# Optimization experiments

Measured on AMD Instinct MI355X. Metric: run time of the kernel, lower is better.

Reference implementation:

```python
import jax, jax.numpy as jnp
import numpy as np

NEURON_CDECAY = 0.5
NEURON_VDECAY = 0.75
NEURON_VTH = 0.5

B, D_IN, T = 4096, 1024, 16
H1, H2, D_OUT = 1024, 1024, 512


def setup_inputs() -> dict:
    key = jax.random.key(0)
    ks = jax.random.split(key, 7)
    def lin(k, fan_in, shape):
        bound = 1.0 / np.sqrt(fan_in)
        return jax.random.uniform(k, shape, jnp.float32, -bound, bound)
    # input spikes: binary-ish spike trains in [0,1)
    in_pop_spikes = (jax.random.uniform(ks[0], (B, D_IN, T)) < 0.3).astype(jnp.float32)
    return {
        "in_pop_spikes": in_pop_spikes,
        "W1": lin(ks[1], D_IN, (H1, D_IN)), "b1": lin(ks[2], D_IN, (H1,)),
        "W2": lin(ks[3], H1, (H2, H1)), "b2": lin(ks[4], H1, (H2,)),
        "Wo": lin(ks[5], H2, (D_OUT, H2)), "bo": lin(ks[6], H2, (D_OUT,)),
        "batch_size": B,
    }


def pseudo_spike(volt):
    return (volt > NEURON_VTH).astype(volt.dtype)


def clif_step(x, W, b, cur, volt, spk):
    cur = cur * NEURON_CDECAY + x @ W.T + b
    volt = volt * NEURON_VDECAY * (1.0 - spk) + cur
    spk = pseudo_spike(volt)
    return cur, volt, spk


def reference(in_pop_spikes, W1, b1, W2, b2, Wo, bo, batch_size):
    bsz = batch_size
    xs = jnp.transpose(in_pop_spikes, (2, 0, 1))  # [T, B, D_in]
    z = lambda d: jnp.zeros((bsz, d), jnp.float32)
    init = (z(H1), z(H1), z(H1), z(H2), z(H2), z(H2), z(D_OUT), z(D_OUT), z(D_OUT))

    def step(state, x):
        c1, v1, s1, c2, v2, s2, co, vo, so = state
        c1, v1, s1 = clif_step(x, W1, b1, c1, v1, s1)
        c2, v2, s2 = clif_step(s1, W2, b2, c2, v2, s2)
        co, vo, so = clif_step(s2, Wo, bo, co, vo, so)
        return (c1, v1, s1, c2, v2, s2, co, vo, so), so

    _, spikes = jax.lax.scan(step, init, xs)  # spikes: [T, B, D_out]
    return jnp.sum(spikes, axis=0) / T
```

## Files before the change

### kernel.cpp

```cpp
#include <hip/hip_runtime.h>


static constexpr int BSZ   = 4096;
static constexpr int D_IN  = 1024;
static constexpr int H1    = 1024;
static constexpr int D_OUT = 512;
static constexpr int M_ROWS = BSZ * 16;

__global__ void pack_x(const float* __restrict__ X, float* __restrict__ A) {
    const int P = blockIdx.x * 256 + threadIdx.x;
    const int b = P >> 10, d = P & 1023;
    const float4* xp = (const float4*)(X + (size_t)P * 16);
    float4 x0 = xp[0], x1 = xp[1], x2 = xp[2], x3 = xp[3];
    const float v[16] = {x0.x, x0.y, x0.z, x0.w, x1.x, x1.y, x1.z, x1.w,
                         x2.x, x2.y, x2.z, x2.w, x3.x, x3.y, x3.z, x3.w};
#pragma unroll
    for (int t = 0; t < 16; ++t)
        A[((size_t)(b * 16 + t)) * 1024 + d] = v[t];
}

__global__ __launch_bounds__(256, 2) void gemm_np(
    const float* __restrict__ A,
    const float* __restrict__ W,
    float* __restrict__ C,
    int N) {
#pragma clang fp contract(off)
    __shared__ float As[32][128];
    __shared__ float Ws[32][128];

    const int tid = threadIdx.x;
    const int tx = tid & 15;
    const int ty = tid >> 4;
    const int m0 = blockIdx.x * 128, n0 = blockIdx.y * 128;

    const int arow = tid & 127, akh = tid >> 7;

    const float* Ab = A + (size_t)(m0 + arow) * 1024 + akh * 16;
    const float* Wb = W + (size_t)(n0 + arow) * 1024 + akh * 16;

    float pacc[8][8] = {};

    for (int kt = 0; kt < 32; ++kt) {
        const int k0 = kt * 32;
        float4 av0 = *(const float4*)(Ab + k0);
        float4 av1 = *(const float4*)(Ab + k0 + 4);
        float4 av2 = *(const float4*)(Ab + k0 + 8);
        float4 av3 = *(const float4*)(Ab + k0 + 12);
        float4 wv0 = *(const float4*)(Wb + k0);
        float4 wv1 = *(const float4*)(Wb + k0 + 4);
        float4 wv2 = *(const float4*)(Wb + k0 + 8);
        float4 wv3 = *(const float4*)(Wb + k0 + 12);
        __syncthreads();
        {
            const float avv[16] = {av0.x, av0.y, av0.z, av0.w,
                                   av1.x, av1.y, av1.z, av1.w,
                                   av2.x, av2.y, av2.z, av2.w,
                                   av3.x, av3.y, av3.z, av3.w};
            const float wvv[16] = {wv0.x, wv0.y, wv0.z, wv0.w,
                                   wv1.x, wv1.y, wv1.z, wv1.w,
                                   wv2.x, wv2.y, wv2.z, wv2.w,
                                   wv3.x, wv3.y, wv3.z, wv3.w};
#pragma unroll
            for (int c = 0; c < 16; ++c) {
                As[akh * 16 + c][arow] = avv[c];
                Ws[akh * 16 + c][arow] = wvv[c];
            }
        }
        __syncthreads();

#pragma unroll
        for (int kk = 0; kk < 32; ++kk) {
            float4 a0 = *(const float4*)&As[kk][ty * 8];
            float4 a1 = *(const float4*)&As[kk][ty * 8 + 4];
            float4 w0 = *(const float4*)&Ws[kk][tx * 4];
            float4 w1 = *(const float4*)&Ws[kk][64 + tx * 4];
            const float a[8] = {a0.x, a0.y, a0.z, a0.w, a1.x, a1.y, a1.z, a1.w};
            const float w[8] = {w0.x, w0.y, w0.z, w0.w, w1.x, w1.y, w1.z, w1.w};
#pragma unroll
            for (int i = 0; i < 8; ++i)
#pragma unroll
                for (int j = 0; j < 8; ++j)
                    pacc[i][j] = __builtin_fmaf(a[i], w[j], pacc[i][j]);
        }
    }

#pragma unroll
    for (int i = 0; i < 8; ++i) {
        float4 s0 = {pacc[i][0], pacc[i][1], pacc[i][2], pacc[i][3]};
        float4 s1 = {pacc[i][4], pacc[i][5], pacc[i][6], pacc[i][7]};
        const size_t r = (size_t)(m0 + ty * 8 + i) * N;
        *(float4*)&C[r + n0 + tx * 4]      = s0;
        *(float4*)&C[r + n0 + 64 + tx * 4] = s1;
    }
}

__global__ void recur_hidden(float* __restrict__ Z, const float* __restrict__ bias) {
#pragma clang fp contract(off)
    const int idx = blockIdx.x * 256 + threadIdx.x;
    const int n = idx & 1023, b = idx >> 10;
    const float bb = bias[n];
    float c = 0.f, v = 0.f, s = 0.f;
#pragma unroll
    for (int t = 0; t < 16; ++t) {
        const size_t p = (size_t)(b * 16 + t) * 1024 + n;
        const float z = Z[p];
        const float t1 = c * 0.5f;
        const float t2 = t1 + z;
        c = t2 + bb;
        const float u1 = v * 0.75f;
        const float u2 = u1 * (1.0f - s);
        v = u2 + c;
        s = (v > 0.5f) ? 1.0f : 0.0f;
        Z[p] = s;
    }
}

__global__ void recur_out(const float* __restrict__ Z, const float* __restrict__ bias,
                          float* __restrict__ Out) {
#pragma clang fp contract(off)
    const int idx = blockIdx.x * 256 + threadIdx.x;
    const int n = idx & 511, b = idx >> 9;
    const float bb = bias[n];
    float c = 0.f, v = 0.f, s = 0.f, acm = 0.f;
#pragma unroll
    for (int t = 0; t < 16; ++t) {
        const float z = Z[(size_t)(b * 16 + t) * 512 + n];
        const float t1 = c * 0.5f;
        const float t2 = t1 + z;
        c = t2 + bb;
        const float u1 = v * 0.75f;
        const float u2 = u1 * (1.0f - s);
        v = u2 + c;
        s = (v > 0.5f) ? 1.0f : 0.0f;
        acm += s;
    }
    Out[(size_t)b * 512 + n] = acm * 0.0625f;
}

extern "C" void kernel_launch(void* const* d_in, const int* in_sizes, int n_in,
                              void* d_out, int out_size, void* d_ws, size_t ws_size,
                              hipStream_t stream) {
    const float* X  = (const float*)d_in[0];
    const float* W1 = (const float*)d_in[1];
    const float* b1 = (const float*)d_in[2];
    const float* W2 = (const float*)d_in[3];
    const float* b2 = (const float*)d_in[4];
    const float* Wo = (const float*)d_in[5];
    const float* bo = (const float*)d_in[6];

    char* ws = (char*)d_ws;
    float* buf0 = (float*)ws;
    float* buf1 = (float*)(ws + (256ull << 20));

    pack_x<<<(BSZ * D_IN) / 256, 256, 0, stream>>>(X, buf0);

    gemm_np<<<dim3(M_ROWS / 128, H1 / 128), 256, 0, stream>>>(buf0, W1, buf1, H1);
    recur_hidden<<<(BSZ * H1) / 256, 256, 0, stream>>>(buf1, b1);
    gemm_np<<<dim3(M_ROWS / 128, H1 / 128), 256, 0, stream>>>(buf1, W2, buf0, H1);
    recur_hidden<<<(BSZ * H1) / 256, 256, 0, stream>>>(buf0, b2);
    gemm_np<<<dim3(M_ROWS / 128, D_OUT / 128), 256, 0, stream>>>(buf0, Wo, buf1, D_OUT);
    recur_out<<<(BSZ * D_OUT) / 256, 256, 0, stream>>>(buf1, bo, (float*)d_out);
}
```

Baseline: 3.890 ms.

## Enlarge GEMM tile to 256x128 with k-major padded and swizzled LDS layout

Result: slower. 4.382 ms (+12.7%).

```diff
diff --git a/kernel.cpp b/kernel.cpp
--- a/kernel.cpp
+++ b/kernel.cpp
@@ -1,5 +1,7 @@
 #include <hip/hip_runtime.h>
 
+
+typedef float floatx4 __attribute__((ext_vector_type(4)));
 
 static constexpr int BSZ   = 4096;
 static constexpr int D_IN  = 1024;
@@ -25,72 +27,77 @@
     float* __restrict__ C,
     int N) {
 #pragma clang fp contract(off)
-    __shared__ float As[32][128];
-    __shared__ float Ws[32][128];
+    __shared__ float As[256 * 33];
+    __shared__ float Ws[128 * 32];
 
     const int tid = threadIdx.x;
     const int tx = tid & 15;
     const int ty = tid >> 4;
-    const int m0 = blockIdx.x * 128, n0 = blockIdx.y * 128;
+    const int m0 = blockIdx.x * 256, n0 = blockIdx.y * 128;
 
-    const int arow = tid & 127, akh = tid >> 7;
+    const float* Ag = A + (size_t)(m0 + tid) * 1024;
+    const int wn = tid & 127, wq0 = (tid >> 7) * 4;
+    const float* Wg = W + (size_t)(n0 + wn) * 1024 + wq0 * 4;
+    const int wswz = (wn >> 3) & 7;
 
-    const float* Ab = A + (size_t)(m0 + arow) * 1024 + akh * 16;
-    const float* Wb = W + (size_t)(n0 + arow) * 1024 + akh * 16;
-
-    float pacc[8][8] = {};
+    float acc[16][8] = {};
 
     for (int kt = 0; kt < 32; ++kt) {
         const int k0 = kt * 32;
-        float4 av0 = *(const float4*)(Ab + k0);
-        float4 av1 = *(const float4*)(Ab + k0 + 4);
-        float4 av2 = *(const float4*)(Ab + k0 + 8);
-        float4 av3 = *(const float4*)(Ab + k0 + 12);
-        float4 wv0 = *(const float4*)(Wb + k0);
-        float4 wv1 = *(const float4*)(Wb + k0 + 4);
-        float4 wv2 = *(const float4*)(Wb + k0 + 8);
-        float4 wv3 = *(const float4*)(Wb + k0 + 12);
+        floatx4 av[8], wv[4];
+#pragma unroll
+        for (int c = 0; c < 8; ++c)
+            av[c] = *(const floatx4*)(Ag + k0 + c * 4);
+#pragma unroll
+        for (int q = 0; q < 4; ++q)
+            wv[q] = *(const floatx4*)(Wg + k0 + q * 4);
         __syncthreads();
-        {
-            const float avv[16] = {av0.x, av0.y, av0.z, av0.w,
-                                   av1.x, av1.y, av1.z, av1.w,
-                                   av2.x, av2.y, av2.z, av2.w,
-                                   av3.x, av3.y, av3.z, av3.w};
-            const float wvv[16] = {wv0.x, wv0.y, wv0.z, wv0.w,
-                                   wv1.x, wv1.y, wv1.z, wv1.w,
-                                   wv2.x, wv2.y, wv2.z, wv2.w,
-                                   wv3.x, wv3.y, wv3.z, wv3.w};
 #pragma unroll
-            for (int c = 0; c < 16; ++c) {
-                As[akh * 16 + c][arow] = avv[c];
-                Ws[akh * 16 + c][arow] = wvv[c];
-            }
-        }
+        for (int c = 0; c < 8; ++c)
+            *(floatx4*)&As[tid * 33 + c * 4] = av[c];
+#pragma unroll
+        for (int q = 0; q < 4; ++q)
+            *(floatx4*)&Ws[wn * 32 + (((wq0 + q) ^ wswz) * 4)] = wv[q];
         __syncthreads();
 
 #pragma unroll
-        for (int kk = 0; kk < 32; ++kk) {
-            float4 a0 = *(const float4*)&As[kk][ty * 8];
-            float4 a1 = *(const float4*)&As[kk][ty * 8 + 4];
-            float4 w0 = *(const float4*)&Ws[kk][tx * 4];
-            float4 w1 = *(const float4*)&Ws[kk][64 + tx * 4];
-            const float a[8] = {a0.x, a0.y, a0.z, a0.w, a1.x, a1.y, a1.z, a1.w};
-            const float w[8] = {w0.x, w0.y, w0.z, w0.w, w1.x, w1.y, w1.z, w1.w};
+        for (int kq = 0; kq < 8; ++kq) {
+            const int wch = (kq ^ (tx & 7)) * 4;
+            const int ach = kq * 4;
+            floatx4 w4[8], a4[8];
+#pragma unroll
+            for (int j = 0; j < 8; ++j)
+                w4[j] = *(const floatx4*)&Ws[(tx * 8 + j) * 32 + wch];
 #pragma unroll
             for (int i = 0; i < 8; ++i)
+                a4[i] = *(const floatx4*)&As[(ty * 16 + i) * 33 + ach];
 #pragma unroll
-                for (int j = 0; j < 8; ++j)
-                    pacc[i][j] = __builtin_fmaf(a[i], w[j], pacc[i][j]);
+            for (int kk = 0; kk < 4; ++kk)
+#pragma unroll
+                for (int i = 0; i < 8; ++i)
+#pragma unroll
+                    for (int j = 0; j < 8; ++j)
+                        acc[i][j] = __builtin_fmaf(a4[i][kk], w4[j][kk], acc[i][j]);
+#pragma unroll
+            for (int i = 0; i < 8; ++i)
+                a4[i] = *(const floatx4*)&As[(ty * 16 + 8 + i) * 33 + ach];
+#pragma unroll
+            for (int kk = 0; kk < 4; ++kk)
+#pragma unroll
+                for (int i = 0; i < 8; ++i)
+#pragma unroll
+                    for (int j = 0; j < 8; ++j)
+                        acc[8 + i][j] = __builtin_fmaf(a4[i][kk], w4[j][kk], acc[8 + i][j]);
         }
     }
 
 #pragma unroll
-    for (int i = 0; i < 8; ++i) {
-        float4 s0 = {pacc[i][0], pacc[i][1], pacc[i][2], pacc[i][3]};
-        float4 s1 = {pacc[i][4], pacc[i][5], pacc[i][6], pacc[i][7]};
-        const size_t r = (size_t)(m0 + ty * 8 + i) * N;
-        *(float4*)&C[r + n0 + tx * 4]      = s0;
-        *(float4*)&C[r + n0 + 64 + tx * 4] = s1;
+    for (int i = 0; i < 16; ++i) {
+        floatx4 s0 = {acc[i][0], acc[i][1], acc[i][2], acc[i][3]};
+        floatx4 s1 = {acc[i][4], acc[i][5], acc[i][6], acc[i][7]};
+        float* cp = C + (size_t)(m0 + ty * 16 + i) * N + n0 + tx * 8;
+        *(floatx4*)cp       = s0;
+        *(floatx4*)(cp + 4) = s1;
     }
 }
 
@@ -154,10 +161,10 @@
 
     pack_x<<<(BSZ * D_IN) / 256, 256, 0, stream>>>(X, buf0);
 
-    gemm_np<<<dim3(M_ROWS / 128, H1 / 128), 256, 0, stream>>>(buf0, W1, buf1, H1);
+    gemm_np<<<dim3(M_ROWS / 256, H1 / 128), 256, 0, stream>>>(buf0, W1, buf1, H1);
     recur_hidden<<<(BSZ * H1) / 256, 256, 0, stream>>>(buf1, b1);
-    gemm_np<<<dim3(M_ROWS / 128, H1 / 128), 256, 0, stream>>>(buf1, W2, buf0, H1);
+    gemm_np<<<dim3(M_ROWS / 256, H1 / 128), 256, 0, stream>>>(buf1, W2, buf0, H1);
     recur_hidden<<<(BSZ * H1) / 256, 256, 0, stream>>>(buf0, b2);
-    gemm_np<<<dim3(M_ROWS / 128, D_OUT / 128), 256, 0, stream>>>(buf0, Wo, buf1, D_OUT);
+    gemm_np<<<dim3(M_ROWS / 256, D_OUT / 128), 256, 0, stream>>>(buf0, Wo, buf1, D_OUT);
     recur_out<<<(BSZ * D_OUT) / 256, 256, 0, stream>>>(buf1, bo, (float*)d_out);
 }
```

## Store input and hidden spikes as uint8 and unpack them inside the GEMM

Applied to the files above, without the earlier changes.

After: 3.885 ms. No clear change (-0.1%).

```diff
diff --git a/kernel.cpp b/kernel.cpp
--- a/kernel.cpp
+++ b/kernel.cpp
@@ -7,7 +7,7 @@
 static constexpr int D_OUT = 512;
 static constexpr int M_ROWS = BSZ * 16;
 
-__global__ void pack_x(const float* __restrict__ X, float* __restrict__ A) {
+__global__ void pack_x(const float* __restrict__ X, unsigned char* __restrict__ A8) {
     const int P = blockIdx.x * 256 + threadIdx.x;
     const int b = P >> 10, d = P & 1023;
     const float4* xp = (const float4*)(X + (size_t)P * 16);
@@ -16,17 +16,17 @@
                          x2.x, x2.y, x2.z, x2.w, x3.x, x3.y, x3.z, x3.w};
 #pragma unroll
     for (int t = 0; t < 16; ++t)
-        A[((size_t)(b * 16 + t)) * 1024 + d] = v[t];
+        A8[((size_t)(b * 16 + t)) * 1024 + d] = (unsigned char)v[t];
 }
 
 __global__ __launch_bounds__(256, 2) void gemm_np(
-    const float* __restrict__ A,
+    const unsigned char* __restrict__ A8,
     const float* __restrict__ W,
     float* __restrict__ C,
     int N) {
 #pragma clang fp contract(off)
-    __shared__ float As[32][128];
-    __shared__ float Ws[32][128];
+    __shared__ unsigned As4[8][128];
+    __shared__ float    Ws[32][128];
 
     const int tid = threadIdx.x;
     const int tx = tid & 15;
@@ -35,66 +35,69 @@
 
     const int arow = tid & 127, akh = tid >> 7;
 
-    const float* Ab = A + (size_t)(m0 + arow) * 1024 + akh * 16;
-    const float* Wb = W + (size_t)(n0 + arow) * 1024 + akh * 16;
+    const unsigned char* Ab = A8 + (size_t)(m0 + arow) * 1024 + akh * 16;
+    const float*         Wb = W  + (size_t)(n0 + arow) * 1024 + akh * 16;
 
-    float pacc[8][8] = {};
+    float acc[8][8] = {};
 
     for (int kt = 0; kt < 32; ++kt) {
         const int k0 = kt * 32;
-        float4 av0 = *(const float4*)(Ab + k0);
-        float4 av1 = *(const float4*)(Ab + k0 + 4);
-        float4 av2 = *(const float4*)(Ab + k0 + 8);
-        float4 av3 = *(const float4*)(Ab + k0 + 12);
+        uint4  av  = *(const uint4*)(Ab + k0);
         float4 wv0 = *(const float4*)(Wb + k0);
         float4 wv1 = *(const float4*)(Wb + k0 + 4);
         float4 wv2 = *(const float4*)(Wb + k0 + 8);
         float4 wv3 = *(const float4*)(Wb + k0 + 12);
         __syncthreads();
+        As4[akh * 4 + 0][arow] = av.x;
+        As4[akh * 4 + 1][arow] = av.y;
+        As4[akh * 4 + 2][arow] = av.z;
+        As4[akh * 4 + 3][arow] = av.w;
         {
-            const float avv[16] = {av0.x, av0.y, av0.z, av0.w,
-                                   av1.x, av1.y, av1.z, av1.w,
-                                   av2.x, av2.y, av2.z, av2.w,
-                                   av3.x, av3.y, av3.z, av3.w};
             const float wvv[16] = {wv0.x, wv0.y, wv0.z, wv0.w,
                                    wv1.x, wv1.y, wv1.z, wv1.w,
                                    wv2.x, wv2.y, wv2.z, wv2.w,
                                    wv3.x, wv3.y, wv3.z, wv3.w};
 #pragma unroll
-            for (int c = 0; c < 16; ++c) {
-                As[akh * 16 + c][arow] = avv[c];
+            for (int c = 0; c < 16; ++c)
                 Ws[akh * 16 + c][arow] = wvv[c];
-            }
         }
         __syncthreads();
 
 #pragma unroll
-        for (int kk = 0; kk < 32; ++kk) {
-            float4 a0 = *(const float4*)&As[kk][ty * 8];
-            float4 a1 = *(const float4*)&As[kk][ty * 8 + 4];
-            float4 w0 = *(const float4*)&Ws[kk][tx * 4];
-            float4 w1 = *(const float4*)&Ws[kk][64 + tx * 4];
-            const float a[8] = {a0.x, a0.y, a0.z, a0.w, a1.x, a1.y, a1.z, a1.w};
-            const float w[8] = {w0.x, w0.y, w0.z, w0.w, w1.x, w1.y, w1.z, w1.w};
+        for (int kq = 0; kq < 8; ++kq) {
+            uint4 ap0 = *(const uint4*)&As4[kq][ty * 8];
+            uint4 ap1 = *(const uint4*)&As4[kq][ty * 8 + 4];
+            const unsigned ap[8] = {ap0.x, ap0.y, ap0.z, ap0.w,
+                                    ap1.x, ap1.y, ap1.z, ap1.w};
 #pragma unroll
-            for (int i = 0; i < 8; ++i)
+            for (int kk = 0; kk < 4; ++kk) {
+                float4 w0 = *(const float4*)&Ws[kq * 4 + kk][tx * 4];
+                float4 w1 = *(const float4*)&Ws[kq * 4 + kk][64 + tx * 4];
+                const float w[8] = {w0.x, w0.y, w0.z, w0.w,
+                                    w1.x, w1.y, w1.z, w1.w};
 #pragma unroll
-                for (int j = 0; j < 8; ++j)
-                    pacc[i][j] = __builtin_fmaf(a[i], w[j], pacc[i][j]);
+                for (int i = 0; i < 8; ++i) {
+                    const float ai = (float)((ap[i] >> (8 * kk)) & 0xffu);
+#pragma unroll
+                    for (int j = 0; j < 8; ++j)
+                        acc[i][j] = __builtin_fmaf(ai, w[j], acc[i][j]);
+                }
+            }
         }
     }
 
 #pragma unroll
     for (int i = 0; i < 8; ++i) {
-        float4 s0 = {pacc[i][0], pacc[i][1], pacc[i][2], pacc[i][3]};
-        float4 s1 = {pacc[i][4], pacc[i][5], pacc[i][6], pacc[i][7]};
+        float4 s0 = {acc[i][0], acc[i][1], acc[i][2], acc[i][3]};
+        float4 s1 = {acc[i][4], acc[i][5], acc[i][6], acc[i][7]};
         const size_t r = (size_t)(m0 + ty * 8 + i) * N;
         *(float4*)&C[r + n0 + tx * 4]      = s0;
         *(float4*)&C[r + n0 + 64 + tx * 4] = s1;
     }
 }
 
-__global__ void recur_hidden(float* __restrict__ Z, const float* __restrict__ bias) {
+__global__ void recur_hidden(const float* __restrict__ Z, const float* __restrict__ bias,
+                             unsigned char* __restrict__ S8) {
 #pragma clang fp contract(off)
     const int idx = blockIdx.x * 256 + threadIdx.x;
     const int n = idx & 1023, b = idx >> 10;
@@ -111,7 +114,7 @@
         const float u2 = u1 * (1.0f - s);
         v = u2 + c;
         s = (v > 0.5f) ? 1.0f : 0.0f;
-        Z[p] = s;
+        S8[p] = (unsigned char)s;
     }
 }
 
@@ -149,15 +152,17 @@
     const float* bo = (const float*)d_in[6];
 
     char* ws = (char*)d_ws;
-    float* buf0 = (float*)ws;
-    float* buf1 = (float*)(ws + (256ull << 20));
+    unsigned char* A8  = (unsigned char*)ws;
+    unsigned char* S81 = (unsigned char*)(ws + ( 64ull << 20));
+    unsigned char* S82 = (unsigned char*)(ws + (128ull << 20));
+    float*         Zf  = (float*)(ws + (192ull << 20));
 
-    pack_x<<<(BSZ * D_IN) / 256, 256, 0, stream>>>(X, buf0);
+    pack_x<<<(BSZ * D_IN) / 256, 256, 0, stream>>>(X, A8);
 
-    gemm_np<<<dim3(M_ROWS / 128, H1 / 128), 256, 0, stream>>>(buf0, W1, buf1, H1);
-    recur_hidden<<<(BSZ * H1) / 256, 256, 0, stream>>>(buf1, b1);
-    gemm_np<<<dim3(M_ROWS / 128, H1 / 128), 256, 0, stream>>>(buf1, W2, buf0, H1);
-    recur_hidden<<<(BSZ * H1) / 256, 256, 0, stream>>>(buf0, b2);
-    gemm_np<<<dim3(M_ROWS / 128, D_OUT / 128), 256, 0, stream>>>(buf0, Wo, buf1, D_OUT);
-    recur_out<<<(BSZ * D_OUT) / 256, 256, 0, stream>>>(buf1, bo, (float*)d_out);
+    gemm_np<<<dim3(M_ROWS / 128, H1 / 128), 256, 0, stream>>>(A8, W1, Zf, H1);
+    recur_hidden<<<(BSZ * H1) / 256, 256, 0, stream>>>(Zf, b1, S81);
+    gemm_np<<<dim3(M_ROWS / 128, H1 / 128), 256, 0, stream>>>(S81, W2, Zf, H1);
+    recur_hidden<<<(BSZ * H1) / 256, 256, 0, stream>>>(Zf, b2, S82);
+    gemm_np<<<dim3(M_ROWS / 128, D_OUT / 128), 256, 0, stream>>>(S82, Wo, Zf, D_OUT);
+    recur_out<<<(BSZ * D_OUT) / 256, 256, 0, stream>>>(Zf, bo, (float*)d_out);
 }
```
